# Kernel tuning notes

Measured on AMD Instinct MI355X. Metric: run time of the kernel, lower is better.

## Reference

```python
import jax, jax.numpy as jnp
import numpy as np

IN_FEATURES = 16080
TREES = 64
LEAVES = 128
CLASSES = 16
BATCH = 64


def setup_inputs() -> dict:
    key = jax.random.key(0)
    k_x, k_w, k_b, k_c = jax.random.split(key, 4)
    x = jax.random.normal(k_x, (BATCH, TREES, IN_FEATURES), dtype=jnp.float32)
    # nn.Linear(16080, leaves): weight [leaves, in], bias [leaves]
    lim = 1.0 / np.sqrt(IN_FEATURES)
    W = jax.random.uniform(k_w, (LEAVES, IN_FEATURES), minval=-lim, maxval=lim, dtype=jnp.float32)
    b = jax.random.uniform(k_b, (LEAVES,), minval=-lim, maxval=lim, dtype=jnp.float32)
    # contribution parameter ~ U(-1, 1), shape [trees, leaves, classes]
    contribution = jax.random.uniform(k_c, (TREES, LEAVES, CLASSES), minval=-1.0, maxval=1.0, dtype=jnp.float32)
    return {"x": x, "W": W, "b": b, "contribution": contribution}


def reference(x, W, b, contribution):
    # Linear + Hardtanh: [B, T, L]
    symbolic_paths = jnp.clip(jnp.einsum('bti,li->btl', x, W) + b, -1.0, 1.0)
    # Fused form of the per-(tree,leaf) outer-product loop: [B, T, L, C]
    class_value = symbolic_paths[..., None] * contribution[None]
    p = jax.nn.softmax(class_value, axis=-1)
    # 1 - sum(p^2) over classes (Gini-style impurity): [B, T, L]
    class_value = jnp.sum(1.0 - p * p, axis=-1)
    return (symbolic_paths, class_value)
```

## Files before the change

kernel.cpp:

```cpp
#include <hip/hip_runtime.h>
#include <hip/hip_bf16.h>
#include <stdint.h>

#define IN_F   16080
#define NTREES 64
#define NLEAF  128
#define NCLS   16
#define NBATCH 64
#define M_TOT  (NBATCH*NTREES)
#define OUT_HALF (M_TOT*NLEAF)

#define BM 64
#define BN 128
#define BK 64
#define KSPLIT 16
#define NSTEPS ((IN_F + BK - 1)/BK)

typedef __attribute__((ext_vector_type(8))) short short8;
typedef __attribute__((ext_vector_type(4))) float f32x4;

typedef const __attribute__((address_space(1))) uint32_t gu32_t;
typedef __attribute__((address_space(3))) uint32_t su32_t;

__device__ __forceinline__ short8 cvt8(float4 lo, float4 hi){
  union { short8 s8; __hip_bfloat162 h2[4]; } u;
  u.h2[0] = __float22bfloat162_rn(make_float2(lo.x, lo.y));
  u.h2[1] = __float22bfloat162_rn(make_float2(lo.z, lo.w));
  u.h2[2] = __float22bfloat162_rn(make_float2(hi.x, hi.y));
  u.h2[3] = __float22bfloat162_rn(make_float2(hi.z, hi.w));
  return u.s8;
}

__global__ __launch_bounds__(256)
void wcvt_kernel(const float* __restrict__ W, short* __restrict__ Wb){
  int i = (blockIdx.x * 256 + threadIdx.x) << 3;
  float4 a = *(const float4*)(W + i);
  float4 b = *(const float4*)(W + i + 4);
  *(short8*)(Wb + i) = cvt8(a, b);
}

__global__ __launch_bounds__(256, 4)
void gemm_slab_kernel(const float* __restrict__ X,
                      const short* __restrict__ Wb,
                      float* __restrict__ accbuf,
                      const short* __restrict__ zeropage){
  __shared__ __align__(16) short BsH[NLEAF * BK];

  const int tid = threadIdx.x;
  const int m0  = blockIdx.x * BM;
  const int kc  = blockIdx.y;
  const int s0  = (kc * NSTEPS) / KSPLIT;
  const int s1  = ((kc + 1) * NSTEPS) / KSPLIT;

  const int lane = tid & 63;
  const int wv   = tid >> 6;
  const int wm   = wv & 1;
  const int wn   = wv >> 1;
  const int fr   = lane & 15;
  const int fq   = lane >> 4;

  f32x4 acc[2][4];
  #pragma unroll
  for (int mt = 0; mt < 2; ++mt)
    #pragma unroll
    for (int nt = 0; nt < 4; ++nt) acc[mt][nt] = (f32x4){0.f,0.f,0.f,0.f};

  for (int s = s0; s < s1; ++s){
    const int k0 = s * BK;
    __syncthreads();

    float4 av[2][2][2];
    #pragma unroll
    for (int mt = 0; mt < 2; ++mt){
      const float* rowp = X + (size_t)(m0 + wm*32 + mt*16 + fr) * IN_F;
      #pragma unroll
      for (int h = 0; h < 2; ++h)
        #pragma unroll
        for (int q = 0; q < 2; ++q){
          int gk = k0 + h*32 + fq*8 + q*4;
          av[mt][h][q] = (gk + 4 <= IN_F) ? *(const float4*)(rowp + gk)
                                          : make_float4(0.f,0.f,0.f,0.f);
        }
    }

    #pragma unroll
    for (int j = 0; j < 4; ++j){
      int lin = j*256 + tid;
      int r   = lin >> 3;
      int p   = lin & 7;
      int c   = p ^ (r & 7);
      int gk  = k0 + (c << 3);
      const short* gp = (gk + 8 <= IN_F) ? (Wb + (size_t)r * IN_F + gk)
                                         : zeropage;
      __builtin_amdgcn_global_load_lds((gu32_t*)gp, (su32_t*)(BsH + lin*8),
                                       16, 0, 0);
    }

    short8 af[2][2];
    #pragma unroll
    for (int mt = 0; mt < 2; ++mt)
      #pragma unroll
      for (int h = 0; h < 2; ++h)
        af[mt][h] = cvt8(av[mt][h][0], av[mt][h][1]);

    __syncthreads();

    #pragma unroll
    for (int nt = 0; nt < 4; ++nt){
      const int l  = wn*64 + nt*16 + fr;
      const int xw = l & 7;
      const short* rowb = BsH + l*BK;
      #pragma unroll
      for (int h = 0; h < 2; ++h){
        int cc = (((h << 2) + fq) ^ xw) << 3;
        short8 bf = *(const short8*)(rowb + cc);
        #pragma unroll
        for (int mt = 0; mt < 2; ++mt)
          acc[mt][nt] = __builtin_amdgcn_mfma_f32_16x16x32_bf16(
                            af[mt][h], bf, acc[mt][nt], 0, 0, 0);
      }
    }
  }

  #pragma unroll
  for (int mt = 0; mt < 2; ++mt){
    const int rbase = m0 + wm*32 + mt*16 + fq*4;
    #pragma unroll
    for (int nt = 0; nt < 4; ++nt){
      int col = wn*64 + nt*16 + fr;
      #pragma unroll
      for (int r = 0; r < 4; ++r)
        accbuf[(size_t)kc * OUT_HALF + (size_t)(rbase + r) * NLEAF + col]
            = acc[mt][nt][r];
    }
  }
}

__global__ __launch_bounds__(256)
void epilogue_slab_kernel(const float* __restrict__ slabs,
                          float* __restrict__ out,
                          const float* __restrict__ bias,
                          const float* __restrict__ contrib){
  int idx = blockIdx.x * 256 + threadIdx.x;
  int l   = idx & (NLEAF - 1);
  int row = idx >> 7;
  int t   = row & (NTREES - 1);

  float s = 0.f;
  #pragma unroll
  for (int kc = 0; kc < KSPLIT; ++kc)
    s += slabs[(size_t)kc * OUT_HALF + idx];
  s += bias[l];
  s = fminf(1.f, fmaxf(-1.f, s));
  out[idx] = s;

  const float4* cp = (const float4*)(contrib + (((size_t)t * NLEAF + l) << 4));
  float4 c0 = cp[0], c1 = cp[1], c2 = cp[2], c3 = cp[3];
  float v[16] = { s*c0.x, s*c0.y, s*c0.z, s*c0.w,
                  s*c1.x, s*c1.y, s*c1.z, s*c1.w,
                  s*c2.x, s*c2.y, s*c2.z, s*c2.w,
                  s*c3.x, s*c3.y, s*c3.z, s*c3.w };
  float m = v[0];
  #pragma unroll
  for (int c = 1; c < 16; ++c) m = fmaxf(m, v[c]);
  float se = 0.f, se2 = 0.f;
  #pragma unroll
  for (int c = 0; c < 16; ++c){
    float e = __expf(v[c] - m);
    se  += e;
    se2 += e * e;
  }
  out[OUT_HALF + idx] = (float)NCLS - se2 / (se * se);
}

__global__ __launch_bounds__(256, 4)
void gemm_atomic_kernel(const float* __restrict__ X,
                        const float* __restrict__ Wg,
                        float* __restrict__ accbuf,
                        const float* __restrict__ zeropage){
  __shared__ __align__(16) float BsF[BN * BK];

  const int tid = threadIdx.x;
  const int m0  = blockIdx.x * BM;
  const int kc  = blockIdx.y;
  const int s0  = (kc * NSTEPS) / KSPLIT;
  const int s1  = ((kc + 1) * NSTEPS) / KSPLIT;

  const int lane = tid & 63;
  const int wv   = tid >> 6;
  const int wm   = wv & 1;
  const int wn   = wv >> 1;
  const int fr   = lane & 15;
  const int fq   = lane >> 4;

  f32x4 acc[2][4];
  #pragma unroll
  for (int mt = 0; mt < 2; ++mt)
    #pragma unroll
    for (int nt = 0; nt < 4; ++nt) acc[mt][nt] = (f32x4){0.f,0.f,0.f,0.f};

  for (int s = s0; s < s1; ++s){
    const int k0 = s * BK;
    __syncthreads();

    float4 av[2][2][2];
    #pragma unroll
    for (int mt = 0; mt < 2; ++mt){
      const float* rowp = X + (size_t)(m0 + wm*32 + mt*16 + fr) * IN_F;
      #pragma unroll
      for (int h = 0; h < 2; ++h)
        #pragma unroll
        for (int q = 0; q < 2; ++q){
          int gk = k0 + h*32 + fq*8 + q*4;
          av[mt][h][q] = (gk + 4 <= IN_F) ? *(const float4*)(rowp + gk)
                                          : make_float4(0.f,0.f,0.f,0.f);
        }
    }

    #pragma unroll
    for (int j = 0; j < 8; ++j){
      int lin = j*256 + tid;
      int r   = lin >> 4;
      int p   = lin & 15;
      int c   = p ^ (r & 7);
      int gk  = k0 + c*4;
      const float* gp = (gk + 4 <= IN_F) ? (Wg + (size_t)r * IN_F + gk)
                                         : zeropage;
      __builtin_amdgcn_global_load_lds((gu32_t*)gp, (su32_t*)(BsF + lin*4),
                                       16, 0, 0);
    }

    short8 af[2][2];
    #pragma unroll
    for (int mt = 0; mt < 2; ++mt)
      #pragma unroll
      for (int h = 0; h < 2; ++h)
        af[mt][h] = cvt8(av[mt][h][0], av[mt][h][1]);

    __syncthreads();

    #pragma unroll
    for (int nt = 0; nt < 4; ++nt){
      const int l  = wn*64 + nt*16 + fr;
      const int xw = l & 7;
      const float* rowb = BsF + l*64;
      #pragma unroll
      for (int h = 0; h < 2; ++h){
        int c0 = h*8 + fq*2;
        float4 b0 = *(const float4*)(rowb + ((c0    ) ^ xw)*4);
        float4 b1 = *(const float4*)(rowb + ((c0 + 1) ^ xw)*4);
        short8 bf = cvt8(b0, b1);
        #pragma unroll
        for (int mt = 0; mt < 2; ++mt)
          acc[mt][nt] = __builtin_amdgcn_mfma_f32_16x16x32_bf16(
                            af[mt][h], bf, acc[mt][nt], 0, 0, 0);
      }
    }
  }

  #pragma unroll
  for (int mt = 0; mt < 2; ++mt){
    const int rbase = m0 + wm*32 + mt*16 + fq*4;
    #pragma unroll
    for (int nt = 0; nt < 4; ++nt){
      int col = wn*64 + nt*16 + fr;
      #pragma unroll
      for (int r = 0; r < 4; ++r)
        atomicAdd(&accbuf[(size_t)(rbase + r) * NLEAF + col], acc[mt][nt][r]);
    }
  }
}

__global__ __launch_bounds__(256)
void epilogue_inplace_kernel(float* __restrict__ out,
                             const float* __restrict__ bias,
                             const float* __restrict__ contrib){
  int idx = blockIdx.x * 256 + threadIdx.x;
  int l   = idx & (NLEAF - 1);
  int row = idx >> 7;
  int t   = row & (NTREES - 1);

  float s = out[idx] + bias[l];
  s = fminf(1.f, fmaxf(-1.f, s));
  out[idx] = s;

  const float4* cp = (const float4*)(contrib + (((size_t)t * NLEAF + l) << 4));
  float4 c0 = cp[0], c1 = cp[1], c2 = cp[2], c3 = cp[3];
  float v[16] = { s*c0.x, s*c0.y, s*c0.z, s*c0.w,
                  s*c1.x, s*c1.y, s*c1.z, s*c1.w,
                  s*c2.x, s*c2.y, s*c2.z, s*c2.w,
                  s*c3.x, s*c3.y, s*c3.z, s*c3.w };
  float m = v[0];
  #pragma unroll
  for (int c = 1; c < 16; ++c) m = fmaxf(m, v[c]);
  float se = 0.f, se2 = 0.f;
  #pragma unroll
  for (int c = 0; c < 16; ++c){
    float e = __expf(v[c] - m);
    se  += e;
    se2 += e * e;
  }
  out[OUT_HALF + idx] = (float)NCLS - se2 / (se * se);
}

extern "C" void kernel_launch(void* const* d_in, const int* in_sizes, int n_in,
                              void* d_out, int out_size, void* d_ws, size_t ws_size,
                              hipStream_t stream){
  const float* X       = (const float*)d_in[0];
  const float* Wg      = (const float*)d_in[1];
  const float* bias    = (const float*)d_in[2];
  const float* contrib = (const float*)d_in[3];
  float* out = (float*)d_out;

  const size_t SLAB_BYTES = (size_t)KSPLIT * OUT_HALF * sizeof(float);
  const size_t WB_BYTES   = (size_t)NLEAF * IN_F * sizeof(short);
  char* ws = (char*)d_ws;
  const int WCVT_BLOCKS = (NLEAF * IN_F) / (256 * 8);

  dim3 g1(M_TOT / BM, KSPLIT);

  if (ws_size >= SLAB_BYTES + WB_BYTES + 256){
    float* slabs = (float*)ws;
    short* Wb    = (short*)(ws + SLAB_BYTES);
    short* zp    = (short*)(ws + SLAB_BYTES + WB_BYTES);
    hipMemsetAsync(zp, 0, 256, stream);
    wcvt_kernel<<<WCVT_BLOCKS, 256, 0, stream>>>(Wg, Wb);
    gemm_slab_kernel<<<g1, 256, 0, stream>>>(X, Wb, slabs, zp);
    epilogue_slab_kernel<<<OUT_HALF / 256, 256, 0, stream>>>(slabs, out, bias, contrib);
  } else {
    hipMemsetAsync(out, 0, (size_t)OUT_HALF * sizeof(float), stream);
    hipMemsetAsync(ws, 0, 256, stream);
    gemm_atomic_kernel<<<g1, 256, 0, stream>>>(X, Wg, out, (const float*)ws);
    epilogue_inplace_kernel<<<OUT_HALF / 256, 256, 0, stream>>>(out, bias, contrib);
  }
}
```

Measured before the change: 410.9 us.

## Double-buffer W tiles in LDS and prefetch next X/W slab in GEMM loop

Converts the split-K GEMM main loop to a software pipeline: the W tile is double-buffered in LDS, and both the next W tile (async global_load_lds) and the next X registers are issued before the current tile's MFMAs run. A partial vmcnt wait plus barrier replaces the two full __syncthreads per step, aiming to hide global load latency behind compute. It doubles LDS use, which may reduce occupancy, and it relies on the vmcnt count matching the outstanding loads. The last iteration also prefetches past the slice end, which costs extra loads.

```diff
diff --git a/kernel.cpp b/kernel.cpp
--- a/kernel.cpp
+++ b/kernel.cpp
@@ -44,7 +44,7 @@
                       const short* __restrict__ Wb,
                       float* __restrict__ accbuf,
                       const short* __restrict__ zeropage){
-  __shared__ __align__(16) short BsH[NLEAF * BK];
+  __shared__ __align__(16) short BsH[2][NLEAF * BK];
 
   const int tid = threadIdx.x;
   const int m0  = blockIdx.x * BM;
@@ -65,36 +65,58 @@
     #pragma unroll
     for (int nt = 0; nt < 4; ++nt) acc[mt][nt] = (f32x4){0.f,0.f,0.f,0.f};
 
-  for (int s = s0; s < s1; ++s){
-    const int k0 = s * BK;
-    __syncthreads();
-
-    float4 av[2][2][2];
-    #pragma unroll
-    for (int mt = 0; mt < 2; ++mt){
-      const float* rowp = X + (size_t)(m0 + wm*32 + mt*16 + fr) * IN_F;
-      #pragma unroll
-      for (int h = 0; h < 2; ++h)
-        #pragma unroll
-        for (int q = 0; q < 2; ++q){
-          int gk = k0 + h*32 + fq*8 + q*4;
-          av[mt][h][q] = (gk + 4 <= IN_F) ? *(const float4*)(rowp + gk)
-                                          : make_float4(0.f,0.f,0.f,0.f);
-        }
-    }
-
+  float4 av[2][2][2];
+  const float* arow[2];
+  arow[0] = X + (size_t)(m0 + wm*32 + 0*16 + fr) * IN_F;
+  arow[1] = X + (size_t)(m0 + wm*32 + 1*16 + fr) * IN_F;
+
+  {
+    const int k0 = s0 * BK;
     #pragma unroll
     for (int j = 0; j < 4; ++j){
       int lin = j*256 + tid;
       int r   = lin >> 3;
-      int p   = lin & 7;
-      int c   = p ^ (r & 7);
+      int c   = (lin & 7) ^ (r & 7);
       int gk  = k0 + (c << 3);
       const short* gp = (gk + 8 <= IN_F) ? (Wb + (size_t)r * IN_F + gk)
                                          : zeropage;
-      __builtin_amdgcn_global_load_lds((gu32_t*)gp, (su32_t*)(BsH + lin*8),
+      __builtin_amdgcn_global_load_lds((gu32_t*)gp, (su32_t*)(&BsH[0][0] + lin*8),
                                        16, 0, 0);
     }
+    #pragma unroll
+    for (int mt = 0; mt < 2; ++mt)
+      #pragma unroll
+      for (int h = 0; h < 2; ++h)
+        #pragma unroll
+        for (int q = 0; q < 2; ++q){
+          int gk = k0 + h*32 + fq*8 + q*4;
+          av[mt][h][q] = (gk + 4 <= IN_F) ? *(const float4*)(arow[mt] + gk)
+                                          : make_float4(0.f,0.f,0.f,0.f);
+        }
+  }
+
+  for (int s = s0; s < s1; ++s){
+    const int par = (s - s0) & 1;
+    short* bcur = &BsH[par][0];
+    short* bnxt = &BsH[par ^ 1][0];
+
+    {
+      const int k1 = (s + 1) * BK;
+      #pragma unroll
+      for (int j = 0; j < 4; ++j){
+        int lin = j*256 + tid;
+        int r   = lin >> 3;
+        int c   = (lin & 7) ^ (r & 7);
+        int gk  = k1 + (c << 3);
+        const short* gp = (gk + 8 <= IN_F) ? (Wb + (size_t)r * IN_F + gk)
+                                           : zeropage;
+        __builtin_amdgcn_global_load_lds((gu32_t*)gp, (su32_t*)(bnxt + lin*8),
+                                         16, 0, 0);
+      }
+    }
+
+    asm volatile("s_waitcnt vmcnt(4)" ::: "memory");
+    __builtin_amdgcn_s_barrier();
 
     short8 af[2][2];
     #pragma unroll
@@ -103,13 +125,25 @@
       for (int h = 0; h < 2; ++h)
         af[mt][h] = cvt8(av[mt][h][0], av[mt][h][1]);
 
-    __syncthreads();
+    {
+      const int k1 = (s + 1) * BK;
+      #pragma unroll
+      for (int mt = 0; mt < 2; ++mt)
+        #pragma unroll
+        for (int h = 0; h < 2; ++h)
+          #pragma unroll
+          for (int q = 0; q < 2; ++q){
+            int gk = k1 + h*32 + fq*8 + q*4;
+            av[mt][h][q] = (gk + 4 <= IN_F) ? *(const float4*)(arow[mt] + gk)
+                                            : make_float4(0.f,0.f,0.f,0.f);
+          }
+    }
 
     #pragma unroll
     for (int nt = 0; nt < 4; ++nt){
       const int l  = wn*64 + nt*16 + fr;
       const int xw = l & 7;
-      const short* rowb = BsH + l*BK;
+      const short* rowb = bcur + l*BK;
       #pragma unroll
       for (int h = 0; h < 2; ++h){
         int cc = (((h << 2) + fq) ^ xw) << 3;
@@ -120,6 +154,8 @@
                             af[mt][h], bf, acc[mt][nt], 0, 0, 0);
       }
     }
+
+    __builtin_amdgcn_s_barrier();
   }
 
   #pragma unroll
```

After: 400.5 us. 2.5% less time.
